# Kernel tuning notes

Hardware: AMD Instinct MI355X
Metric: run time of the kernel (lower is better)

## Reference

```python
import jax, jax.numpy as jnp
import numpy as np

L = 19                      # blur kernel side
K2 = L * L                  # 361 taps
PAD1 = L // 2               # 9 (left/top)
PAD2 = L // 2               # 9 (right/bottom, l odd)


def _sv_blur(x, kernel):
    """Spatially-varying blur: out[b,c,i,j] = sum_k patch_k(x)[b,c,i,j]*kernel[b,k,i,j] / K2.

    Divisor: the torch module always recomputes divisor = fold(unfold(ones)).sum(1)
    (padded size H+18 != 128 init size), and with fold kernel_size=1 this is the
    constant L*L everywhere.
    """
    B, C, H, W = x.shape
    pad = jnp.pad(x, ((0, 0), (0, 0), (PAD1, PAD2), (PAD1, PAD2)), mode='reflect')
    # Extract LxL patches per pixel; single-channel batch of B*C maps, so output
    # channel ordering is row-major over (u, v) kernel offsets, matching torch unfold.
    xr = pad.reshape(B * C, 1, H + PAD1 + PAD2, W + PAD1 + PAD2)
    patches = jax.lax.conv_general_dilated_patches(
        xr, filter_shape=(L, L), window_strides=(1, 1), padding='VALID')  # [B*C, K2, H, W]
    patches = patches.reshape(B, C, K2, H, W)
    out = jnp.einsum('bckhw,bkhw->bchw', patches, kernel)
    return out / jnp.asarray(K2, dtype=out.dtype)


def setup_inputs() -> dict:
    key = jax.random.key(0)
    k1, k2 = jax.random.split(key)
    B, C, H, W = 2, 3, 256, 256
    inp = jax.random.normal(k1, (B, C, H, W), dtype=jnp.float32)
    kernel = jax.random.uniform(k2, (B, K2, H, W), dtype=jnp.float32)
    return {"input": inp, "kernel": kernel}


def reference(input, kernel):
    return _sv_blur(input, kernel)
```

## Files before the change

### kernel.cpp

```cpp
#include <hip/hip_runtime.h>


#define LW     19
#define PAD    9
#define K2     361
#define HH     256
#define WW     256
#define CC     3
#define TILE_W 64
#define TILE_H 4
#define SM_W   (TILE_W + LW - 1)
#define SM_H   (TILE_H + LW - 1)

__global__ __launch_bounds__(256)
void svblur_kernel(const float* __restrict__ x,
                   const float* __restrict__ ker,
                   float* __restrict__ out) {
    __shared__ float tile[CC][SM_H][SM_W];

    const int tx  = threadIdx.x;
    const int ty  = threadIdx.y;
    const int tid = ty * TILE_W + tx;
    const int j0  = blockIdx.x * TILE_W;
    const int i0  = blockIdx.y * TILE_H;
    const int b   = blockIdx.z;

    const float* xb = x + (size_t)b * CC * HH * WW;
    for (int idx = tid; idx < CC * SM_H * SM_W; idx += 256) {
        int c  = idx / (SM_H * SM_W);
        int rm = idx - c * (SM_H * SM_W);
        int r  = rm / SM_W;
        int cc = rm - r * SM_W;
        int gr = i0 + r - PAD;
        gr = gr < 0 ? -gr : (gr >= HH ? 2 * HH - 2 - gr : gr);
        int gc = j0 + cc - PAD;
        gc = gc < 0 ? -gc : (gc >= WW ? 2 * WW - 2 - gc : gc);
        ((float*)tile)[idx] = xb[((size_t)c * HH + gr) * WW + gc];
    }
    __syncthreads();

    const int i = i0 + ty;
    const int j = j0 + tx;
    const float* kp = ker + ((size_t)b * K2 * HH + i) * WW + j;

    float a0 = 0.f, a1 = 0.f, a2 = 0.f;
    for (int u = 0; u < LW; ++u) {
        const float* r0 = &tile[0][ty + u][tx];
        const float* r1 = &tile[1][ty + u][tx];
        const float* r2 = &tile[2][ty + u][tx];
        const float* kq = kp + (size_t)(u * LW) * (HH * WW);
        #pragma unroll
        for (int v = 0; v < LW; ++v) {
            float kv = kq[(size_t)v * (HH * WW)];
            a0 = fmaf(r0[v], kv, a0);
            a1 = fmaf(r1[v], kv, a1);
            a2 = fmaf(r2[v], kv, a2);
        }
    }

    const float s = 1.0f / (float)K2;
    float* op = out + (((size_t)b * CC) * HH + i) * WW + j;
    op[0 * (HH * WW)] = a0 * s;
    op[1 * (HH * WW)] = a1 * s;
    op[2 * (HH * WW)] = a2 * s;
}

extern "C" void kernel_launch(void* const* d_in, const int* in_sizes, int n_in,
                              void* d_out, int out_size, void* d_ws, size_t ws_size,
                              hipStream_t stream) {
    const float* x   = (const float*)d_in[0];
    const float* ker = (const float*)d_in[1];
    float* out       = (float*)d_out;

    dim3 grid(WW / TILE_W, HH / TILE_H, 2);
    dim3 block(TILE_W, TILE_H, 1);
    svblur_kernel<<<grid, block, 0, stream>>>(x, ker, out);
}
```

Baseline: 264.0 us.

## Split kernel rows across blocks with atomic accumulation and float4 register tiling

```diff
diff --git a/kernel.cpp b/kernel.cpp
--- a/kernel.cpp
+++ b/kernel.cpp
@@ -7,62 +7,100 @@
 #define HH     256
 #define WW     256
 #define CC     3
-#define TILE_W 64
-#define TILE_H 4
-#define SM_W   (TILE_W + LW - 1)
-#define SM_H   (TILE_H + LW - 1)
+#define HW     (HH * WW)
 
-__global__ __launch_bounds__(256)
-void svblur_kernel(const float* __restrict__ x,
-                   const float* __restrict__ ker,
-                   float* __restrict__ out) {
-    __shared__ float tile[CC][SM_H][SM_W];
+#define TX     16
+#define TY     8
+#define TPW    4
+#define TILE_W (TX * TPW)
+#define NCHUNK 5
+#define USZ    4
+#define RHALO  (TY + USZ - 1)
+#define SM_W   84
 
-    const int tx  = threadIdx.x;
-    const int ty  = threadIdx.y;
-    const int tid = ty * TILE_W + tx;
-    const int j0  = blockIdx.x * TILE_W;
-    const int i0  = blockIdx.y * TILE_H;
-    const int b   = blockIdx.z;
+__global__ __launch_bounds__(128)
+void svblur_zero(float* __restrict__ out) {
+    int idx = blockIdx.x * 128 + threadIdx.x;
+    ((float4*)out)[idx] = make_float4(0.f, 0.f, 0.f, 0.f);
+}
 
-    const float* xb = x + (size_t)b * CC * HH * WW;
-    for (int idx = tid; idx < CC * SM_H * SM_W; idx += 256) {
-        int c  = idx / (SM_H * SM_W);
-        int rm = idx - c * (SM_H * SM_W);
+__global__ __launch_bounds__(128)
+void svblur_main(const float* __restrict__ x,
+                 const float* __restrict__ ker,
+                 float* __restrict__ out) {
+    __shared__ float tile[CC][RHALO][SM_W];
+
+    const int tx    = threadIdx.x;
+    const int ty    = threadIdx.y;
+    const int tid   = ty * TX + tx;
+    const int j0    = blockIdx.x * TILE_W;
+    const int i0    = blockIdx.y * TY;
+    const int bz    = blockIdx.z;
+    const int b     = bz / NCHUNK;
+    const int chunk = bz - b * NCHUNK;
+    const int u0    = chunk * USZ;
+    const int usz   = (chunk == NCHUNK - 1) ? (LW - u0) : USZ;
+
+    const float* xb = x + (size_t)b * CC * HW;
+    for (int idx = tid; idx < CC * RHALO * SM_W; idx += TX * TY) {
+        int c  = idx / (RHALO * SM_W);
+        int rm = idx - c * (RHALO * SM_W);
         int r  = rm / SM_W;
         int cc = rm - r * SM_W;
-        int gr = i0 + r - PAD;
+        int gr = i0 + u0 + r - PAD;
         gr = gr < 0 ? -gr : (gr >= HH ? 2 * HH - 2 - gr : gr);
         int gc = j0 + cc - PAD;
         gc = gc < 0 ? -gc : (gc >= WW ? 2 * WW - 2 - gc : gc);
-        ((float*)tile)[idx] = xb[((size_t)c * HH + gr) * WW + gc];
+        ((float*)tile)[idx] = xb[(c * HH + gr) * WW + gc];
     }
     __syncthreads();
 
-    const int i = i0 + ty;
-    const int j = j0 + tx;
-    const float* kp = ker + ((size_t)b * K2 * HH + i) * WW + j;
+    const int jt = tx * TPW;
+    const int i  = i0 + ty;
+    const int j  = j0 + jt;
 
-    float a0 = 0.f, a1 = 0.f, a2 = 0.f;
-    for (int u = 0; u < LW; ++u) {
-        const float* r0 = &tile[0][ty + u][tx];
-        const float* r1 = &tile[1][ty + u][tx];
-        const float* r2 = &tile[2][ty + u][tx];
-        const float* kq = kp + (size_t)(u * LW) * (HH * WW);
+    float acc[CC][TPW];
+    #pragma unroll
+    for (int c = 0; c < CC; ++c)
+        #pragma unroll
+        for (int p = 0; p < TPW; ++p) acc[c][p] = 0.f;
+
+    for (int uu = 0; uu < usz; ++uu) {
+        float xr[CC][24];
+        #pragma unroll
+        for (int c = 0; c < CC; ++c) {
+            const float4* rp = (const float4*)&tile[c][ty + uu][jt];
+            #pragma unroll
+            for (int q = 0; q < 6; ++q) {
+                float4 v4 = rp[q];
+                xr[c][q * 4 + 0] = v4.x;
+                xr[c][q * 4 + 1] = v4.y;
+                xr[c][q * 4 + 2] = v4.z;
+                xr[c][q * 4 + 3] = v4.w;
+            }
+        }
+        const float4* kb4 = (const float4*)(ker
+            + (size_t)(b * K2 + (u0 + uu) * LW) * HW + (size_t)i * WW + j);
         #pragma unroll
         for (int v = 0; v < LW; ++v) {
-            float kv = kq[(size_t)v * (HH * WW)];
-            a0 = fmaf(r0[v], kv, a0);
-            a1 = fmaf(r1[v], kv, a1);
-            a2 = fmaf(r2[v], kv, a2);
+            float4 kv = kb4[(size_t)v * (HW / 4)];
+            #pragma unroll
+            for (int c = 0; c < CC; ++c) {
+                acc[c][0] = fmaf(xr[c][v + 0], kv.x, acc[c][0]);
+                acc[c][1] = fmaf(xr[c][v + 1], kv.y, acc[c][1]);
+                acc[c][2] = fmaf(xr[c][v + 2], kv.z, acc[c][2]);
+                acc[c][3] = fmaf(xr[c][v + 3], kv.w, acc[c][3]);
+            }
         }
     }
 
     const float s = 1.0f / (float)K2;
-    float* op = out + (((size_t)b * CC) * HH + i) * WW + j;
-    op[0 * (HH * WW)] = a0 * s;
-    op[1 * (HH * WW)] = a1 * s;
-    op[2 * (HH * WW)] = a2 * s;
+    #pragma unroll
+    for (int c = 0; c < CC; ++c) {
+        float* op = out + ((size_t)(b * CC + c) * HH + i) * WW + j;
+        #pragma unroll
+        for (int p = 0; p < TPW; ++p) atomicAdd(op + p, acc[c][p] * s);
+    }
 }
 
 extern "C" void kernel_launch(void* const* d_in, const int* in_sizes, int n_in,
@@ -72,7 +110,9 @@
     const float* ker = (const float*)d_in[1];
     float* out       = (float*)d_out;
 
-    dim3 grid(WW / TILE_W, HH / TILE_H, 2);
-    dim3 block(TILE_W, TILE_H, 1);
-    svblur_kernel<<<grid, block, 0, stream>>>(x, ker, out);
+    svblur_zero<<<393216 / 4 / 128, 128, 0, stream>>>(out);
+
+    dim3 grid(WW / TILE_W, HH / TY, 2 * NCHUNK);
+    dim3 block(TX, TY, 1);
+    svblur_main<<<grid, block, 0, stream>>>(x, ker, out);
 }
```

Result: slower. 279.1 us (+5.7%).
